# Kernel tuning notes

Hardware: AMD Instinct MI355X
Metric: run time of the kernel (lower is better)

Reference implementation:

```python
import jax, jax.numpy as jnp
import numpy as np

NUM_EMBEDDINGS = 2048
EMBEDDING_DIM = 128
BETA = 0.25


def setup_inputs() -> dict:
    key = jax.random.key(0)
    k1, k2 = jax.random.split(key)
    z = jax.random.normal(k1, (64, 32, 32, EMBEDDING_DIM), dtype=jnp.float32)
    # nn.Embedding init: uniform(-1/K, 1/K)
    emb = jax.random.uniform(k2, (NUM_EMBEDDINGS, EMBEDDING_DIM), dtype=jnp.float32,
                             minval=-1.0 / NUM_EMBEDDINGS, maxval=1.0 / NUM_EMBEDDINGS)
    return {"z": z, "emb": emb}


def reference(z, emb):
    beta = BETA
    flat = z.reshape(-1, EMBEDDING_DIM)  # [N, D]
    dist = (jnp.sum(flat * flat, axis=1, keepdims=True)
            - 2.0 * flat @ emb.T
            + jnp.sum(emb * emb, axis=1))
    indices = jnp.argmin(dist, axis=1)  # [N]
    quantized = emb[indices].reshape(z.shape)
    # commitment / codebook loss
    loss = (jnp.mean((jax.lax.stop_gradient(quantized) - z) ** 2)
            + beta * jnp.mean((quantized - jax.lax.stop_gradient(z)) ** 2))
    # straight-through estimator
    quantized_st = z + jax.lax.stop_gradient(quantized - z)
    indices_out = indices.reshape(z.shape[0], -1)
    return quantized_st, indices_out, loss
```

## Files before the change

### kernel.cpp

```cpp
#include <hip/hip_runtime.h>

#define NUM_EMB 2048
#define DIM     128
#define NVEC    65536
#define MARGIN  1.0e-3f
#define CAP     32
#define CHUNK   256
#define NCHUNK  (NUM_EMB / CHUNK)
#define ES      136
#define ZS      132

typedef float  f32x4 __attribute__((ext_vector_type(4)));
typedef short  s16x8 __attribute__((ext_vector_type(8)));

__device__ __forceinline__ ushort f2bf(float f) {
    unsigned u = __float_as_uint(f);
    u = (u + 0x7fffu + ((u >> 16) & 1u)) >> 16;
    return (ushort)u;
}

__device__ __forceinline__ float np_pairwise_sumsq_128(const float* __restrict__ p)
{
    float r[8];
    #pragma unroll
    for (int j = 0; j < 8; ++j) { float v = p[j]; r[j] = __fmul_rn(v, v); }
    #pragma unroll
    for (int i = 8; i < 128; i += 8)
        #pragma unroll
        for (int j = 0; j < 8; ++j) { float v = p[i + j]; r[j] = __fadd_rn(r[j], __fmul_rn(v, v)); }
    float s01 = __fadd_rn(r[0], r[1]);
    float s23 = __fadd_rn(r[2], r[3]);
    float s45 = __fadd_rn(r[4], r[5]);
    float s67 = __fadd_rn(r[6], r[7]);
    return __fadd_rn(__fadd_rn(s01, s23), __fadd_rn(s45, s67));
}

__device__ __forceinline__ float dot_seg(const float4* __restrict__ zp,
                                         const float4* __restrict__ ep,
                                         int seg, float dot)
{
    float4 e[8], zz[8];
    #pragma unroll
    for (int i = 0; i < 8; ++i) { e[i] = ep[seg * 8 + i]; zz[i] = zp[seg * 8 + i]; }
    #pragma unroll
    for (int i = 0; i < 8; ++i) {
        dot = fmaf(zz[i].x, e[i].x, dot);
        dot = fmaf(zz[i].y, e[i].y, dot);
        dot = fmaf(zz[i].z, e[i].z, dot);
        dot = fmaf(zz[i].w, e[i].w, dot);
    }
    return dot;
}

__global__ __launch_bounds__(256)
void prep_kernel(const float* __restrict__ emb,
                 float* __restrict__ enorm,
                 float* __restrict__ accum,
                 unsigned* __restrict__ cand_cnt,
                 ushort* __restrict__ emb_bf)
{
    int g = blockIdx.x * 256 + threadIdx.x;
    cand_cnt[g] = 0u;
    if (g == 0) *accum = 0.0f;

    float4 v = ((const float4*)emb)[g];
    ushort4 b;
    b.x = f2bf(v.x); b.y = f2bf(v.y); b.z = f2bf(v.z); b.w = f2bf(v.w);
    ((ushort4*)emb_bf)[g] = b;

    if (g < NUM_EMB)
        enorm[g] = np_pairwise_sumsq_128(emb + (size_t)g * DIM);
}

__global__ __launch_bounds__(1024, 8)
void approx_kernel(const float* __restrict__ z,
                   const ushort* __restrict__ emb_bf,
                   const float* __restrict__ enorm,
                   unsigned* __restrict__ cand_cnt,
                   ushort* __restrict__ cand)
{
    __shared__ __align__(16) ushort eS[CHUNK * ES];
    __shared__ float cS[CHUNK];
    __shared__ float vS[16][16];

    const int tid  = threadIdx.x;
    const int w    = tid >> 6;
    const int lane = tid & 63;
    const int col  = lane & 15;
    const int quad = lane >> 4;
    const int rg   = w >> 1;
    const int ch   = w & 1;
    const int rowbase = blockIdx.x * 128 + rg * 16;

    s16x8 afrag[4];
    {
        const float* zr = z + (size_t)(rowbase + col) * DIM;
        #pragma unroll
        for (int kt = 0; kt < 4; ++kt) {
            const float4* p = (const float4*)(zr + kt * 32 + quad * 8);
            float4 f0 = p[0], f1 = p[1];
            s16x8 a;
            a[0] = (short)f2bf(f0.x); a[1] = (short)f2bf(f0.y);
            a[2] = (short)f2bf(f0.z); a[3] = (short)f2bf(f0.w);
            a[4] = (short)f2bf(f1.x); a[5] = (short)f2bf(f1.y);
            a[6] = (short)f2bf(f1.z); a[7] = (short)f2bf(f1.w);
            afrag[kt] = a;
        }
    }

    const ushort* eH = eS + ch * 128 * ES;
    const float*  cH = cS + ch * 128;

    float vmax[4], thr[4];
    #pragma unroll
    for (int r = 0; r < 4; ++r) { vmax[r] = -3.0e38f; thr[r] = 3.0e38f; }

    for (int vis = 0; vis < 9; ++vis) {
        const int c = (vis == 0) ? 0 : (vis - 1);
        __syncthreads();

        if (vis > 0) {
            #pragma unroll
            for (int r = 0; r < 4; ++r) {
                float v = fmaxf(vmax[r], vS[w ^ 1][quad * 4 + r]);
                vmax[r] = v;
                thr[r]  = v - 0.5f * MARGIN;
            }
        }

        const uint4* src = (const uint4*)(emb_bf + (size_t)c * CHUNK * DIM);
        #pragma unroll
        for (int i = 0; i < 4; ++i) {
            int li   = i * 1024 + tid;
            int code = li >> 4, fc = li & 15;
            *(uint4*)&eS[code * ES + fc * 8] = src[li];
        }
        if (tid < CHUNK) cS[tid] = -0.5f * enorm[c * CHUNK + tid];
        __syncthreads();

        #pragma unroll 4
        for (int t = 0; t < 8; ++t) {
            s16x8 bfrag[4];
            #pragma unroll
            for (int kt = 0; kt < 4; ++kt)
                bfrag[kt] = *(const s16x8*)&eH[(t * 16 + col) * ES + kt * 32 + quad * 8];

            float h = cH[t * 16 + col];
            f32x4 a = {h, h, h, h};
            #pragma unroll
            for (int kt = 0; kt < 4; ++kt)
                a = __builtin_amdgcn_mfma_f32_16x16x32_bf16(afrag[kt], bfrag[kt], a, 0, 0, 0);

            const int code_g = c * CHUNK + ch * 128 + t * 16 + col;
            #pragma unroll
            for (int r = 0; r < 4; ++r) {
                float v = a[r];
                vmax[r] = fmaxf(vmax[r], v);
                if (vis > 0 && v >= thr[r]) {
                    int row_g = rowbase + quad * 4 + r;
                    unsigned pos = atomicAdd(&cand_cnt[row_g], 1u);
                    if (pos < CAP) cand[(size_t)row_g * CAP + pos] = (ushort)code_g;
                }
            }
        }

        #pragma unroll
        for (int r = 0; r < 4; ++r) {
            float v = vmax[r];
            v = fmaxf(v, __shfl_xor(v, 1, 64));
            v = fmaxf(v, __shfl_xor(v, 2, 64));
            v = fmaxf(v, __shfl_xor(v, 4, 64));
            v = fmaxf(v, __shfl_xor(v, 8, 64));
            vmax[r] = v;
            thr[r]  = v - 0.5f * MARGIN;
        }
        if (col == 0) {
            #pragma unroll
            for (int r = 0; r < 4; ++r)
                vS[w][quad * 4 + r] = vmax[r];
        }
    }
}

__global__ __launch_bounds__(256)
void rerank_kernel(const float* __restrict__ z,
                   const float* __restrict__ emb,
                   const float* __restrict__ enorm,
                   const unsigned* __restrict__ cand_cnt,
                   const ushort* __restrict__ cand,
                   float* __restrict__ out_q,
                   float* __restrict__ out_idx_f,
                   float* __restrict__ accum)
{
    __shared__ float zs[64 * ZS];
    __shared__ float As[64];
    __shared__ int   bidx[64];
    __shared__ int   ovf_list[64];
    __shared__ int   ovf_n;
    __shared__ float rv[4];
    __shared__ int   rvi[4];
    __shared__ float wsum[4];

    const int tid = threadIdx.x;
    const int m0  = blockIdx.x * 64;
    if (tid == 0) ovf_n = 0;

    #pragma unroll
    for (int i = 0; i < 8; ++i) {
        int li = tid + i * 256;
        int m  = li >> 5, dc = li & 31;
        float4 v = ((const float4*)(z + (size_t)(m0 + m) * DIM))[dc];
        *(float4*)&zs[m * ZS + dc * 4] = v;
    }
    __syncthreads();
    if (tid < 64) As[tid] = np_pairwise_sumsq_128(&zs[tid * ZS]);
    __syncthreads();

    const int row_l = tid >> 2;
    const int sub   = tid & 3;
    const int row_g = m0 + row_l;
    const unsigned cnt = cand_cnt[row_g];
    const float A = As[row_l];
    const float4* zp = (const float4*)&zs[row_l * ZS];

    float bv = 3.0e38f;
    int   bi = 0x7fffffff;

    if (cnt <= CAP) {
        for (unsigned ci = sub; ci < cnt; ci += 4) {
            int j = (int)cand[(size_t)row_g * CAP + ci];
            const float4* ep = (const float4*)(emb + (size_t)j * DIM);
            float dot = 0.0f;
            #pragma unroll
            for (int seg = 0; seg < 4; ++seg) dot = dot_seg(zp, ep, seg, dot);
            float t1 = fmaf(-2.0f, dot, A);
            float s  = __fadd_rn(t1, enorm[j]);
            if (s < bv || (s == bv && j < bi)) { bv = s; bi = j; }
        }
    }
    #pragma unroll
    for (int off = 1; off <= 2; off <<= 1) {
        float v  = __shfl_xor(bv, off, 64);
        int   ix = __shfl_xor(bi, off, 64);
        if (v < bv || (v == bv && ix < bi)) { bv = v; bi = ix; }
    }
    if (sub == 0) {
        if (cnt <= CAP) bidx[row_l] = bi;
        else { int p = atomicAdd(&ovf_n, 1); ovf_list[p] = row_l; }
    }
    __syncthreads();

    const int n_ovf = ovf_n;
    for (int o = 0; o < n_ovf; ++o) {
        const int rl = ovf_list[o];
        const float Ar = As[rl];
        const float4* zp2 = (const float4*)&zs[rl * ZS];
        float bv2 = 3.0e38f;
        int   bi2 = 0x7fffffff;
        for (int jj = 0; jj < 8; ++jj) {
            int j = tid * 8 + jj;
            const float4* ep = (const float4*)(emb + (size_t)j * DIM);
            float dot = 0.0f;
            #pragma unroll
            for (int seg = 0; seg < 4; ++seg) dot = dot_seg(zp2, ep, seg, dot);
            float t1 = fmaf(-2.0f, dot, Ar);
            float s  = __fadd_rn(t1, enorm[j]);
            if (s < bv2) { bv2 = s; bi2 = j; }
        }
        #pragma unroll
        for (int off = 1; off < 64; off <<= 1) {
            float v  = __shfl_xor(bv2, off, 64);
            int   ix = __shfl_xor(bi2, off, 64);
            if (v < bv2 || (v == bv2 && ix < bi2)) { bv2 = v; bi2 = ix; }
        }
        if ((tid & 63) == 0) { rv[tid >> 6] = bv2; rvi[tid >> 6] = bi2; }
        __syncthreads();
        if (tid == 0) {
            float fv = rv[0]; int fi = rvi[0];
            #pragma unroll
            for (int ww = 1; ww < 4; ++ww) {
                if (rv[ww] < fv || (rv[ww] == fv && rvi[ww] < fi)) { fv = rv[ww]; fi = rvi[ww]; }
            }
            bidx[rl] = fi;
        }
        __syncthreads();
    }

    if (tid < 64) out_idx_f[m0 + tid] = (float)bidx[tid];

    float part = 0.0f;
    #pragma unroll
    for (int i = 0; i < 8; ++i) {
        int li = tid + i * 256;
        int m  = li >> 5, dc = li & 31;
        int j  = bidx[m];
        float4 q  = ((const float4*)(emb + (size_t)j * DIM))[dc];
        float4 zv = *(const float4*)&zs[m * ZS + dc * 4];
        float4 o;
        o.x = __fadd_rn(zv.x, __fsub_rn(q.x, zv.x));
        o.y = __fadd_rn(zv.y, __fsub_rn(q.y, zv.y));
        o.z = __fadd_rn(zv.z, __fsub_rn(q.z, zv.z));
        o.w = __fadd_rn(zv.w, __fsub_rn(q.w, zv.w));
        ((float4*)out_q)[(size_t)(m0 + m) * 32 + dc] = o;
        float dx = q.x - zv.x, dy = q.y - zv.y, dz = q.z - zv.z, dw = q.w - zv.w;
        part += dx * dx + dy * dy + dz * dz + dw * dw;
    }
    #pragma unroll
    for (int off = 32; off > 0; off >>= 1)
        part += __shfl_down(part, off, 64);
    if ((tid & 63) == 0) wsum[tid >> 6] = part;
    __syncthreads();
    if (tid == 0) atomicAdd(accum, wsum[0] + wsum[1] + wsum[2] + wsum[3]);
}

__global__ void finalize_kernel(const float* __restrict__ accum,
                                float* __restrict__ out_loss)
{
    *out_loss = 1.25f * (*accum) / 8388608.0f;
}

extern "C" void kernel_launch(void* const* d_in, const int* in_sizes, int n_in,
                              void* d_out, int out_size, void* d_ws, size_t ws_size,
                              hipStream_t stream)
{
    const float* z   = (const float*)d_in[0];
    const float* emb = (const float*)d_in[1];
    float* out = (float*)d_out;

    char*     ws       = (char*)d_ws;
    float*    enorm    = (float*)ws;
    float*    accum    = (float*)(ws + 8192);
    unsigned* cand_cnt = (unsigned*)(ws + 16384);
    ushort*   cand     = (ushort*)(ws + 16384 + 262144);
    ushort*   emb_bf   = (ushort*)(ws + 16384 + 262144 + 4194304);

    prep_kernel   <<<NVEC / 256, 256,  0, stream>>>(emb, enorm, accum, cand_cnt, emb_bf);
    approx_kernel <<<NVEC / 128, 1024, 0, stream>>>(z, emb_bf, enorm, cand_cnt, cand);
    rerank_kernel <<<NVEC / 64,  256,  0, stream>>>(z, emb, enorm, cand_cnt, cand,
                                                    out, out + 8388608, accum);
    finalize_kernel<<<1, 1, 0, stream>>>(accum, out + 8388608 + 65536);
}
```

Measured before the change: 244.5 us.

## Prefetch codebook chunks into registers and buffer candidates in shared memory

Loads the next bf16 codebook chunk and its norms into registers while the current chunk is being processed, so global-load latency overlaps the MFMA work; the redundant reload and barrier on the repeated first chunk are skipped. Candidate counters and lists move from global atomics into shared-memory atomics and are written out with one coalesced store per block, which removes the zeroing of the global counters in prep. Costs are extra registers for the prefetch buffer and extra LDS, which may reduce occupancy.

```diff
diff --git a/kernel.cpp b/kernel.cpp
--- a/kernel.cpp
+++ b/kernel.cpp
@@ -56,11 +56,9 @@
 void prep_kernel(const float* __restrict__ emb,
                  float* __restrict__ enorm,
                  float* __restrict__ accum,
-                 unsigned* __restrict__ cand_cnt,
                  ushort* __restrict__ emb_bf)
 {
     int g = blockIdx.x * 256 + threadIdx.x;
-    cand_cnt[g] = 0u;
     if (g == 0) *accum = 0.0f;
 
     float4 v = ((const float4*)emb)[g];
@@ -82,6 +80,8 @@
     __shared__ __align__(16) ushort eS[CHUNK * ES];
     __shared__ float cS[CHUNK];
     __shared__ float vS[16][16];
+    __shared__ __align__(16) ushort candS[128 * CAP];
+    __shared__ unsigned cntS[128];
 
     const int tid  = threadIdx.x;
     const int w    = tid >> 6;
@@ -91,6 +91,8 @@
     const int rg   = w >> 1;
     const int ch   = w & 1;
     const int rowbase = blockIdx.x * 128 + rg * 16;
+
+    if (tid < 128) cntS[tid] = 0u;
 
     s16x8 afrag[4];
     {
@@ -115,9 +117,34 @@
     #pragma unroll
     for (int r = 0; r < 4; ++r) { vmax[r] = -3.0e38f; thr[r] = 3.0e38f; }
 
+    uint4 rbuf[4];
+    float cbuf;
+    {
+        const uint4* src = (const uint4*)emb_bf;
+        #pragma unroll
+        for (int i = 0; i < 4; ++i) rbuf[i] = src[i * 1024 + tid];
+        cbuf = (tid < CHUNK) ? enorm[tid] : 0.0f;
+    }
+
     for (int vis = 0; vis < 9; ++vis) {
         const int c = (vis == 0) ? 0 : (vis - 1);
+
         __syncthreads();
+
+        if (vis != 1) {
+            #pragma unroll
+            for (int i = 0; i < 4; ++i) {
+                int li = i * 1024 + tid, code = li >> 4, fc = li & 15;
+                *(uint4*)&eS[code * ES + fc * 8] = rbuf[i];
+            }
+            if (tid < CHUNK) cS[tid] = -0.5f * cbuf;
+        }
+        if (vis >= 1 && vis <= 7) {
+            const uint4* src = (const uint4*)(emb_bf + (size_t)vis * CHUNK * DIM);
+            #pragma unroll
+            for (int i = 0; i < 4; ++i) rbuf[i] = src[i * 1024 + tid];
+            if (tid < CHUNK) cbuf = enorm[vis * CHUNK + tid];
+        }
 
         if (vis > 0) {
             #pragma unroll
@@ -128,15 +155,7 @@
             }
         }
 
-        const uint4* src = (const uint4*)(emb_bf + (size_t)c * CHUNK * DIM);
-        #pragma unroll
-        for (int i = 0; i < 4; ++i) {
-            int li   = i * 1024 + tid;
-            int code = li >> 4, fc = li & 15;
-            *(uint4*)&eS[code * ES + fc * 8] = src[li];
-        }
-        if (tid < CHUNK) cS[tid] = -0.5f * enorm[c * CHUNK + tid];
-        __syncthreads();
+        if (vis != 1) __syncthreads();
 
         #pragma unroll 4
         for (int t = 0; t < 8; ++t) {
@@ -157,9 +176,9 @@
                 float v = a[r];
                 vmax[r] = fmaxf(vmax[r], v);
                 if (vis > 0 && v >= thr[r]) {
-                    int row_g = rowbase + quad * 4 + r;
-                    unsigned pos = atomicAdd(&cand_cnt[row_g], 1u);
-                    if (pos < CAP) cand[(size_t)row_g * CAP + pos] = (ushort)code_g;
+                    int row_l = rg * 16 + quad * 4 + r;
+                    unsigned pos = atomicAdd(&cntS[row_l], 1u);
+                    if (pos < CAP) candS[row_l * CAP + pos] = (ushort)code_g;
                 }
             }
         }
@@ -180,6 +199,11 @@
                 vS[w][quad * 4 + r] = vmax[r];
         }
     }
+
+    __syncthreads();
+    if (tid < 128) cand_cnt[blockIdx.x * 128 + tid] = cntS[tid];
+    if (tid < 512)
+        ((uint4*)(cand + (size_t)blockIdx.x * 128 * CAP))[tid] = ((const uint4*)candS)[tid];
 }
 
 __global__ __launch_bounds__(256)
@@ -334,7 +358,7 @@
     ushort*   cand     = (ushort*)(ws + 16384 + 262144);
     ushort*   emb_bf   = (ushort*)(ws + 16384 + 262144 + 4194304);
 
-    prep_kernel   <<<NVEC / 256, 256,  0, stream>>>(emb, enorm, accum, cand_cnt, emb_bf);
+    prep_kernel   <<<NVEC / 256, 256,  0, stream>>>(emb, enorm, accum, emb_bf);
     approx_kernel <<<NVEC / 128, 1024, 0, stream>>>(z, emb_bf, enorm, cand_cnt, cand);
     rerank_kernel <<<NVEC / 64,  256,  0, stream>>>(z, emb, enorm, cand_cnt, cand,
                                                     out, out + 8388608, accum);
```

New measurement: 266.2 us. 1.09x slower.

## Give each wave full codebook chunks and count candidates in shared memory

Applied to the files above, without the earlier changes.

Each wave now owns 16 rows and scans every code, instead of two waves splitting each chunk and swapping maxima through shared memory. Chunks double to 512 codes, and the separate first warm-up pass over chunk 0 is replaced by an in-loop running max on the first chunk. Candidate counters become shared-memory atomics that are written out at the end, so prep no longer zeroes them. The trade-off is a larger LDS footprint per block, which lowers occupancy, plus extra shuffles in the first chunk and a looser threshold early in the scan, which may produce more candidates.

```diff
diff --git a/kernel.cpp b/kernel.cpp
--- a/kernel.cpp
+++ b/kernel.cpp
@@ -5,7 +5,7 @@
 #define NVEC    65536
 #define MARGIN  1.0e-3f
 #define CAP     32
-#define CHUNK   256
+#define CHUNK   512
 #define NCHUNK  (NUM_EMB / CHUNK)
 #define ES      136
 #define ZS      132
@@ -56,11 +56,9 @@
 void prep_kernel(const float* __restrict__ emb,
                  float* __restrict__ enorm,
                  float* __restrict__ accum,
-                 unsigned* __restrict__ cand_cnt,
                  ushort* __restrict__ emb_bf)
 {
     int g = blockIdx.x * 256 + threadIdx.x;
-    cand_cnt[g] = 0u;
     if (g == 0) *accum = 0.0f;
 
     float4 v = ((const float4*)emb)[g];
@@ -72,7 +70,7 @@
         enorm[g] = np_pairwise_sumsq_128(emb + (size_t)g * DIM);
 }
 
-__global__ __launch_bounds__(1024, 8)
+__global__ __launch_bounds__(1024, 4)
 void approx_kernel(const float* __restrict__ z,
                    const ushort* __restrict__ emb_bf,
                    const float* __restrict__ enorm,
@@ -81,16 +79,16 @@
 {
     __shared__ __align__(16) ushort eS[CHUNK * ES];
     __shared__ float cS[CHUNK];
-    __shared__ float vS[16][16];
+    __shared__ unsigned cntS[256];
 
     const int tid  = threadIdx.x;
     const int w    = tid >> 6;
     const int lane = tid & 63;
     const int col  = lane & 15;
     const int quad = lane >> 4;
-    const int rg   = w >> 1;
-    const int ch   = w & 1;
-    const int rowbase = blockIdx.x * 128 + rg * 16;
+    const int rowbase = blockIdx.x * 256 + w * 16;
+
+    if (tid < 256) cntS[tid] = 0u;
 
     s16x8 afrag[4];
     {
@@ -108,78 +106,80 @@
         }
     }
 
-    const ushort* eH = eS + ch * 128 * ES;
-    const float*  cH = cS + ch * 128;
-
     float vmax[4], thr[4];
     #pragma unroll
     for (int r = 0; r < 4; ++r) { vmax[r] = -3.0e38f; thr[r] = 3.0e38f; }
 
-    for (int vis = 0; vis < 9; ++vis) {
-        const int c = (vis == 0) ? 0 : (vis - 1);
+    for (int vis = 0; vis < NCHUNK; ++vis) {
+        if (vis > 0) __syncthreads();
+
+        const uint4* src = (const uint4*)(emb_bf + (size_t)vis * CHUNK * DIM);
+        #pragma unroll
+        for (int i = 0; i < 8; ++i) {
+            int li = i * 1024 + tid;
+            int code = li >> 4, fc = li & 15;
+            *(uint4*)&eS[code * ES + fc * 8] = src[li];
+        }
+        if (tid < CHUNK) cS[tid] = -0.5f * enorm[vis * CHUNK + tid];
         __syncthreads();
 
+        #pragma unroll 4
+        for (int t = 0; t < 32; ++t) {
+            s16x8 bfrag[4];
+            #pragma unroll
+            for (int kt = 0; kt < 4; ++kt)
+                bfrag[kt] = *(const s16x8*)&eS[(t * 16 + col) * ES + kt * 32 + quad * 8];
+
+            float h = cS[t * 16 + col];
+            f32x4 a = {h, h, h, h};
+            #pragma unroll
+            for (int kt = 0; kt < 4; ++kt)
+                a = __builtin_amdgcn_mfma_f32_16x16x32_bf16(afrag[kt], bfrag[kt], a, 0, 0, 0);
+
+            #pragma unroll
+            for (int r = 0; r < 4; ++r) vmax[r] = fmaxf(vmax[r], a[r]);
+
+            if (vis == 0) {
+                #pragma unroll
+                for (int r = 0; r < 4; ++r) {
+                    float v = vmax[r];
+                    v = fmaxf(v, __shfl_xor(v, 1, 64));
+                    v = fmaxf(v, __shfl_xor(v, 2, 64));
+                    v = fmaxf(v, __shfl_xor(v, 4, 64));
+                    v = fmaxf(v, __shfl_xor(v, 8, 64));
+                    vmax[r] = v;
+                    thr[r]  = v - 0.5f * MARGIN;
+                }
+            }
+
+            const int code_g = vis * CHUNK + t * 16 + col;
+            #pragma unroll
+            for (int r = 0; r < 4; ++r) {
+                if (a[r] >= thr[r]) {
+                    int row_l = w * 16 + quad * 4 + r;
+                    unsigned pos = atomicAdd(&cntS[row_l], 1u);
+                    if (pos < CAP)
+                        cand[(size_t)(blockIdx.x * 256 + row_l) * CAP + pos] = (ushort)code_g;
+                }
+            }
+        }
+
         if (vis > 0) {
             #pragma unroll
             for (int r = 0; r < 4; ++r) {
-                float v = fmaxf(vmax[r], vS[w ^ 1][quad * 4 + r]);
+                float v = vmax[r];
+                v = fmaxf(v, __shfl_xor(v, 1, 64));
+                v = fmaxf(v, __shfl_xor(v, 2, 64));
+                v = fmaxf(v, __shfl_xor(v, 4, 64));
+                v = fmaxf(v, __shfl_xor(v, 8, 64));
                 vmax[r] = v;
                 thr[r]  = v - 0.5f * MARGIN;
             }
         }
-
-        const uint4* src = (const uint4*)(emb_bf + (size_t)c * CHUNK * DIM);
-        #pragma unroll
-        for (int i = 0; i < 4; ++i) {
-            int li   = i * 1024 + tid;
-            int code = li >> 4, fc = li & 15;
-            *(uint4*)&eS[code * ES + fc * 8] = src[li];
-        }
-        if (tid < CHUNK) cS[tid] = -0.5f * enorm[c * CHUNK + tid];
-        __syncthreads();
-
-        #pragma unroll 4
-        for (int t = 0; t < 8; ++t) {
-            s16x8 bfrag[4];
-            #pragma unroll
-            for (int kt = 0; kt < 4; ++kt)
-                bfrag[kt] = *(const s16x8*)&eH[(t * 16 + col) * ES + kt * 32 + quad * 8];
-
-            float h = cH[t * 16 + col];
-            f32x4 a = {h, h, h, h};
-            #pragma unroll
-            for (int kt = 0; kt < 4; ++kt)
-                a = __builtin_amdgcn_mfma_f32_16x16x32_bf16(afrag[kt], bfrag[kt], a, 0, 0, 0);
-
-            const int code_g = c * CHUNK + ch * 128 + t * 16 + col;
-            #pragma unroll
-            for (int r = 0; r < 4; ++r) {
-                float v = a[r];
-                vmax[r] = fmaxf(vmax[r], v);
-                if (vis > 0 && v >= thr[r]) {
-                    int row_g = rowbase + quad * 4 + r;
-                    unsigned pos = atomicAdd(&cand_cnt[row_g], 1u);
-                    if (pos < CAP) cand[(size_t)row_g * CAP + pos] = (ushort)code_g;
-                }
-            }
-        }
-
-        #pragma unroll
-        for (int r = 0; r < 4; ++r) {
-            float v = vmax[r];
-            v = fmaxf(v, __shfl_xor(v, 1, 64));
-            v = fmaxf(v, __shfl_xor(v, 2, 64));
-            v = fmaxf(v, __shfl_xor(v, 4, 64));
-            v = fmaxf(v, __shfl_xor(v, 8, 64));
-            vmax[r] = v;
-            thr[r]  = v - 0.5f * MARGIN;
-        }
-        if (col == 0) {
-            #pragma unroll
-            for (int r = 0; r < 4; ++r)
-                vS[w][quad * 4 + r] = vmax[r];
-        }
-    }
+    }
+
+    __syncthreads();
+    if (tid < 256) cand_cnt[blockIdx.x * 256 + tid] = cntS[tid];
 }
 
 __global__ __launch_bounds__(256)
@@ -334,8 +334,8 @@
     ushort*   cand     = (ushort*)(ws + 16384 + 262144);
     ushort*   emb_bf   = (ushort*)(ws + 16384 + 262144 + 4194304);
 
-    prep_kernel   <<<NVEC / 256, 256,  0, stream>>>(emb, enorm, accum, cand_cnt, emb_bf);
-    approx_kernel <<<NVEC / 128, 1024, 0, stream>>>(z, emb_bf, enorm, cand_cnt, cand);
+    prep_kernel   <<<NVEC / 256, 256,  0, stream>>>(emb, enorm, accum, emb_bf);
+    approx_kernel <<<NVEC / 256, 1024, 0, stream>>>(z, emb_bf, enorm, cand_cnt, cand);
     rerank_kernel <<<NVEC / 64,  256,  0, stream>>>(z, emb, enorm, cand_cnt, cand,
                                                     out, out + 8388608, accum);
     finalize_kernel<<<1, 1, 0, stream>>>(accum, out + 8388608 + 65536);
```

After: 242.0 us. About the same (-1.0%).
